# Kernel tuning notes

Measured on AMD Instinct MI355X. Metric: run time of the kernel, lower is better.

## Reference

```python
import jax, jax.numpy as jnp
import numpy as np

GRID = 64
AABB_MIN = np.array([-1.25, -1.55, -1.25], dtype=np.float32)
AABB_MAX = np.array([1.25, 0.95, 1.25], dtype=np.float32)
DENSITY_THRESH = 0.5


def setup_inputs() -> dict:
    key = jax.random.key(0)
    ks = jax.random.split(key, 12)
    N, S, H = 8192, 128, 64
    rays_o = jax.random.normal(ks[0], (N, 3), jnp.float32) * 0.1
    d = jax.random.normal(ks[1], (N, 3), jnp.float32)
    rays_d = d / jnp.sqrt(jnp.clip(jnp.sum(d * d, -1, keepdims=True), 1e-20))
    near = 0.05 + jax.random.uniform(ks[2], (N,), jnp.float32) * 0.5
    far = near + 2.0 + jax.random.uniform(ks[3], (N,), jnp.float32) * 0.5
    jitter = jax.random.uniform(ks[4], (N, S), jnp.float32)
    density_field = jax.random.uniform(ks[5], (GRID, GRID, GRID), jnp.float32)
    W1 = jax.random.normal(ks[6], (3, H), jnp.float32) * 0.5
    b1 = jnp.zeros((H,), jnp.float32)
    W2 = jax.random.normal(ks[7], (H, H), jnp.float32) * (1.0 / np.sqrt(H))
    b2 = jnp.zeros((H,), jnp.float32)
    Wsig = jax.random.normal(ks[8], (H, 1), jnp.float32) * (1.0 / np.sqrt(H))
    bsig = jnp.zeros((1,), jnp.float32)
    Wrgb = jax.random.normal(ks[9], (H, 3), jnp.float32) * (1.0 / np.sqrt(H))
    brgb = jnp.zeros((3,), jnp.float32)
    return {"rays_o": rays_o, "rays_d": rays_d, "near": near, "far": far,
            "jitter": jitter, "density_field": density_field,
            "W1": W1, "b1": b1, "W2": W2, "b2": b2,
            "Wsig": Wsig, "bsig": bsig, "Wrgb": Wrgb, "brgb": brgb}


def _render_train(rays_o, rays_d, near, far, jitter, density_field,
                  W1, b1, W2, b2, Wsig, bsig, Wrgb, brgb):
    N, S = jitter.shape
    step = (far - near) / S                                  # [N]
    offset = jnp.asarray(AABB_MIN)
    scale = jnp.asarray(AABB_MAX) - jnp.asarray(AABB_MIN)
    # uniform march (raymarch_train): z_i = near + i*step, zeroed where grid empty
    z = near[:, None] + jnp.arange(S, dtype=jnp.float32)[None, :] * step[:, None]  # [N,S]
    pts0 = rays_o[:, None, :] + z[..., None] * rays_d[:, None, :]                  # [N,S,3]
    u = (pts0 - offset) / scale
    idx = jnp.floor(u * GRID).astype(jnp.int32)
    inb = jnp.all((idx >= 0) & (idx < GRID), axis=-1)
    idxc = jnp.clip(idx, 0, GRID - 1)
    occ = density_field[idxc[..., 0], idxc[..., 1], idxc[..., 2]] > DENSITY_THRESH
    z_vals = jnp.where(occ & inb, z, 0.0)                    # [N,S]
    mask = z_vals > 0
    # stratified jitter (torch: z_vals + rand * step_size)
    z_vals = z_vals + jitter * step[:, None]
    pts = rays_o[:, None, :] + z_vals[..., None] * rays_d[:, None, :]  # [N,S,3]
    # radiance-field MLP (stand-in for `model(pts, None)`)
    h = jax.nn.relu(jnp.einsum('nsc,ch->nsh', pts, W1) + b1)
    h = jax.nn.relu(jnp.einsum('nsh,hk->nsk', h, W2) + b2)
    sigma = (jnp.einsum('nsh,ho->nso', h, Wsig) + bsig)[..., 0]        # [N,S]
    rgb = jax.nn.sigmoid(jnp.einsum('nsh,ho->nso', h, Wrgb) + brgb)    # [N,S,3]
    # torch fills masked-out samples with sigma=-1000, rgb=0
    sigma = jnp.where(mask, sigma, -1000.0)
    rgb = jnp.where(mask[..., None], rgb, 0.0)
    # composite
    dists = jnp.broadcast_to(step[:, None], sigma.shape)
    tau = jax.nn.relu(sigma) * dists
    alpha = 1.0 - jnp.exp(-tau)
    trans = jnp.concatenate([jnp.ones_like(alpha[..., :1]),
                             jnp.cumprod(1.0 - alpha + 1e-10, axis=-1)], axis=-1)
    w = alpha * trans[..., :-1]                              # [N,S]
    no_hit = trans[..., -1]
    color = jnp.sum(w[..., None] * rgb, axis=-2) + no_hit[..., None]   # bg_color=None -> white
    depth = jnp.sum(w * z_vals, axis=-1)
    return color, depth


def reference(rays_o, rays_d, near, far, jitter, density_field,
              W1, b1, W2, b2, Wsig, bsig, Wrgb, brgb):
    color, depth = _render_train(rays_o, rays_d, near, far, jitter, density_field,
                                 W1, b1, W2, b2, Wsig, bsig, Wrgb, brgb)
    return color
```

## Files before the change

kernel.cpp:

```cpp
#include <hip/hip_runtime.h>
#include <math.h>

#define S 128
#define H 64
#define RPB 8
#define SPB (RPB * S)
#define T 256

typedef __attribute__((ext_vector_type(8))) short bf16x8;
typedef __attribute__((ext_vector_type(4))) float f32x4;
#define MFMA16(a, b, c) __builtin_amdgcn_mfma_f32_16x16x32_bf16((a), (b), (c), 0, 0, 0)

__device__ __forceinline__ short f2bf(float x) {
    unsigned u = __float_as_uint(x);
    unsigned r = (u + 0x7fffu + ((u >> 16) & 1u)) >> 16;
    return (short)r;
}

__device__ __forceinline__ bool sample_mask(
    float ox, float oy, float oz, float dx, float dy, float dz,
    float nr, float step, int s, const float* __restrict__ density)
{
    const float z  = __fadd_rn(nr, __fmul_rn((float)s, step));
    const float px = __fadd_rn(ox, __fmul_rn(z, dx));
    const float py = __fadd_rn(oy, __fmul_rn(z, dy));
    const float pz = __fadd_rn(oz, __fmul_rn(z, dz));
    const float gx = floorf(__fmul_rn(__fdiv_rn(__fsub_rn(px, -1.25f), 2.5f), 64.0f));
    const float gy = floorf(__fmul_rn(__fdiv_rn(__fsub_rn(py, -1.55f), 2.5f), 64.0f));
    const float gz = floorf(__fmul_rn(__fdiv_rn(__fsub_rn(pz, -1.25f), 2.5f), 64.0f));
    const int ix = (int)gx, iy = (int)gy, iz = (int)gz;
    const bool inb = (ix >= 0) && (ix < 64) && (iy >= 0) && (iy < 64) &&
                     (iz >= 0) && (iz < 64);
    const int cx = min(max(ix, 0), 63);
    const int cy = min(max(iy, 0), 63);
    const int cz = min(max(iz, 0), 63);
    const float dval = density[(cx << 12) | (cy << 6) | cz];
    return inb && (dval > 0.5f);
}

__global__ __launch_bounds__(256)
void fused_mfma_kernel(const float* __restrict__ rays_o, const float* __restrict__ rays_d,
                       const float* __restrict__ nearv, const float* __restrict__ farv,
                       const float* __restrict__ jitter, const float* __restrict__ density,
                       const float* __restrict__ W1, const float* __restrict__ b1,
                       const float* __restrict__ W2, const float* __restrict__ b2,
                       const float* __restrict__ Wsig, const float* __restrict__ bsig,
                       const float* __restrict__ Wrgb, const float* __restrict__ brgb,
                       float* __restrict__ out, int N)
{
    __shared__ __align__(16) short sW2t[H * 72];
    __shared__ __align__(16) short hX[4][16 * 72];
    __shared__ unsigned short s_list[SPB];
    __shared__ float s_alpha[SPB];
    __shared__ float s_r[SPB], s_g[SPB], s_b[SPB];
    __shared__ int s_wcnt[4];
    __shared__ int s_wbase[4];

    const int tid  = threadIdx.x;
    const int lane = tid & 63;
    const int wv   = tid >> 6;
    const int blk  = blockIdx.x;
    const int mrow = lane & 15;
    const int quad = lane >> 4;

    for (int e = tid; e < H * H; e += T) {
        const int k = e >> 6, n = e & 63;
        sW2t[n * 72 + k] = f2bf(W2[e]);
    }

    const int lbase = tid * 4;
    const int gra   = blk * RPB + (lbase >> 7);
    unsigned int mybits = 0u;
    if (gra < N) {
        const float ox = rays_o[gra * 3 + 0], oy = rays_o[gra * 3 + 1], oz = rays_o[gra * 3 + 2];
        const float dx = rays_d[gra * 3 + 0], dy = rays_d[gra * 3 + 1], dz = rays_d[gra * 3 + 2];
        const float nr = nearv[gra];
        const float step = __fdiv_rn(__fsub_rn(farv[gra], nr), 128.0f);
        const int s0 = lbase & (S - 1);
        #pragma unroll
        for (int j = 0; j < 4; ++j) {
            const bool m = sample_mask(ox, oy, oz, dx, dy, dz, nr, step, s0 + j, density);
            if (m) {
                mybits |= (1u << j);
            } else {
                s_alpha[lbase + j] = 0.0f;
                s_r[lbase + j] = 0.0f;
                s_g[lbase + j] = 0.0f;
                s_b[lbase + j] = 0.0f;
            }
        }
    } else {
        #pragma unroll
        for (int j = 0; j < 4; ++j) {
            s_alpha[lbase + j] = 0.0f;
            s_r[lbase + j] = 0.0f;
            s_g[lbase + j] = 0.0f;
            s_b[lbase + j] = 0.0f;
        }
    }
    const int mycnt = __popc(mybits);
    int inc = mycnt;
    #pragma unroll
    for (int off = 1; off < 64; off <<= 1) {
        const int u = __shfl_up(inc, off, 64);
        if (lane >= off) inc += u;
    }
    if (lane == 63) s_wcnt[wv] = inc;
    __syncthreads();
    if (tid == 0) {
        int t0 = 0;
        #pragma unroll
        for (int i = 0; i < 4; ++i) { s_wbase[i] = t0; t0 += s_wcnt[i]; }
    }
    __syncthreads();
    int pos = s_wbase[wv] + (inc - mycnt);
    #pragma unroll
    for (int j = 0; j < 4; ++j) {
        if ((mybits >> j) & 1u) s_list[pos++] = (unsigned short)(lbase + j);
    }
    __syncthreads();
    const int K = s_wbase[3] + s_wcnt[3];

    bf16x8 w2f[4][2];
    #pragma unroll
    for (int nt = 0; nt < 4; ++nt) {
        #pragma unroll
        for (int ks = 0; ks < 2; ++ks) {
            w2f[nt][ks] = *(const bf16x8*)&sW2t[(mrow + 16 * nt) * 72 + 32 * ks + 8 * quad];
        }
    }
    bf16x8 w1f[4];
    #pragma unroll
    for (int nt = 0; nt < 4; ++nt) {
        bf16x8 f = {0, 0, 0, 0, 0, 0, 0, 0};
        if (quad == 0) {
            const int n = mrow + 16 * nt;
            f[0] = f2bf(W1[n]);
            f[1] = f2bf(W1[64 + n]);
            f[2] = f2bf(W1[128 + n]);
        }
        w1f[nt] = f;
    }
    bf16x8 a3f[2];
    #pragma unroll
    for (int ks = 0; ks < 2; ++ks) {
        bf16x8 f = {0, 0, 0, 0, 0, 0, 0, 0};
        if (mrow < 4) {
            #pragma unroll
            for (int j = 0; j < 8; ++j) {
                const int k = 32 * ks + 8 * quad + j;
                const float v = (mrow == 0) ? Wsig[k] : Wrgb[k * 3 + (mrow - 1)];
                f[j] = f2bf(v);
            }
        }
        a3f[ks] = f;
    }
    float b1v[4], b2v[4];
    #pragma unroll
    for (int nt = 0; nt < 4; ++nt) {
        b1v[nt] = b1[mrow + 16 * nt];
        b2v[nt] = b2[mrow + 16 * nt];
    }
    const float bsg = bsig[0];
    const float br0 = brgb[0], br1 = brgb[1], br2 = brgb[2];

    const f32x4 z4 = {0.f, 0.f, 0.f, 0.f};
    const int ntask = (K + 15) >> 4;
    short* const hb = &hX[wv][0];

    for (int t = wv; t < ntask; t += 4) {
        const int slot = (t << 4) + mrow;
        const bool valid = slot < K;
        const int id = s_list[valid ? slot : 0];
        const int r = blk * RPB + (id >> 7);
        const int s = id & (S - 1);
        const float nr = nearv[r];
        const float step = __fdiv_rn(__fsub_rn(farv[r], nr), 128.0f);
        const float zs = __fadd_rn(nr, __fmul_rn((float)s, step));
        const float zj = zs + jitter[blk * SPB + id] * step;
        const float qx = rays_o[r * 3 + 0] + zj * rays_d[r * 3 + 0];
        const float qy = rays_o[r * 3 + 1] + zj * rays_d[r * 3 + 1];
        const float qz = rays_o[r * 3 + 2] + zj * rays_d[r * 3 + 2];

        bf16x8 ah = {0, 0, 0, 0, 0, 0, 0, 0};
        if (quad == 0) { ah[0] = f2bf(qx); ah[1] = f2bf(qy); ah[2] = f2bf(qz); }
        #pragma unroll
        for (int nt = 0; nt < 4; ++nt) {
            const f32x4 c1 = MFMA16(ah, w1f[nt], z4);
            #pragma unroll
            for (int rg = 0; rg < 4; ++rg) {
                const float v = fmaxf(c1[rg] + b1v[nt], 0.0f);
                hb[(4 * quad + rg) * 72 + mrow + 16 * nt] = f2bf(v);
            }
        }

        bf16x8 a2_0 = *(const bf16x8*)&hb[mrow * 72 + 8 * quad];
        bf16x8 a2_1 = *(const bf16x8*)&hb[mrow * 72 + 32 + 8 * quad];
        #pragma unroll
        for (int nt = 0; nt < 4; ++nt) {
            const f32x4 c2 = MFMA16(a2_1, w2f[nt][1], MFMA16(a2_0, w2f[nt][0], z4));
            #pragma unroll
            for (int rg = 0; rg < 4; ++rg) {
                const float v = fmaxf(c2[rg] + b2v[nt], 0.0f);
                hb[(4 * quad + rg) * 72 + mrow + 16 * nt] = f2bf(v);
            }
        }

        bf16x8 b3_0 = *(const bf16x8*)&hb[mrow * 72 + 8 * quad];
        bf16x8 b3_1 = *(const bf16x8*)&hb[mrow * 72 + 32 + 8 * quad];
        const f32x4 c3 = MFMA16(a3f[1], b3_1, MFMA16(a3f[0], b3_0, z4));

        if (quad == 0 && valid) {
            const float sg = c3[0] + bsg;
            const float tau = fmaxf(sg, 0.0f) * step;
            s_alpha[id] = 1.0f - expf(-tau);
            s_r[id] = 1.0f / (1.0f + expf(-(c3[1] + br0)));
            s_g[id] = 1.0f / (1.0f + expf(-(c3[2] + br1)));
            s_b[id] = 1.0f / (1.0f + expf(-(c3[3] + br2)));
        }
    }
    __syncthreads();

    #pragma unroll
    for (int ri = wv; ri < RPB; ri += 4) {
        const int gr = blk * RPB + ri;
        if (gr >= N) break;
        const int b0 = ri * S + 2 * lane;
        const float2 a01 = *reinterpret_cast<const float2*>(&s_alpha[b0]);
        const float a0 = a01.x, a1 = a01.y;
        const float t0 = (1.0f - a0) + 1e-10f;
        const float t1 = (1.0f - a1) + 1e-10f;
        float v = t0 * t1;
        #pragma unroll
        for (int off = 1; off < 64; off <<= 1) {
            const float u = __shfl_up(v, off, 64);
            if (lane >= off) v *= u;
        }
        float excl = __shfl_up(v, 1, 64);
        if (lane == 0) excl = 1.0f;
        const float no_hit = __shfl(v, 63, 64);
        const float w0 = a0 * excl;
        const float w1 = a1 * (excl * t0);
        const float2 r01 = *reinterpret_cast<const float2*>(&s_r[b0]);
        const float2 g01 = *reinterpret_cast<const float2*>(&s_g[b0]);
        const float2 b01 = *reinterpret_cast<const float2*>(&s_b[b0]);
        float cr = w0 * r01.x + w1 * r01.y;
        float cg = w0 * g01.x + w1 * g01.y;
        float cb = w0 * b01.x + w1 * b01.y;
        #pragma unroll
        for (int off = 32; off >= 1; off >>= 1) {
            cr += __shfl_xor(cr, off, 64);
            cg += __shfl_xor(cg, off, 64);
            cb += __shfl_xor(cb, off, 64);
        }
        if (lane == 0) {
            out[gr * 3 + 0] = cr + no_hit;
            out[gr * 3 + 1] = cg + no_hit;
            out[gr * 3 + 2] = cb + no_hit;
        }
    }
}

extern "C" void kernel_launch(void* const* d_in, const int* in_sizes, int n_in,
                              void* d_out, int out_size, void* d_ws, size_t ws_size,
                              hipStream_t stream) {
    const float* rays_o  = (const float*)d_in[0];
    const float* rays_d  = (const float*)d_in[1];
    const float* nearv   = (const float*)d_in[2];
    const float* farv    = (const float*)d_in[3];
    const float* jitter  = (const float*)d_in[4];
    const float* density = (const float*)d_in[5];
    const float* W1      = (const float*)d_in[6];
    const float* b1      = (const float*)d_in[7];
    const float* W2      = (const float*)d_in[8];
    const float* b2      = (const float*)d_in[9];
    const float* Wsig    = (const float*)d_in[10];
    const float* bsig    = (const float*)d_in[11];
    const float* Wrgb    = (const float*)d_in[12];
    const float* brgb    = (const float*)d_in[13];
    float* out = (float*)d_out;

    const int N = in_sizes[2];

    fused_mfma_kernel<<<dim3((N + RPB - 1) / RPB), dim3(T), 0, stream>>>(
        rays_o, rays_d, nearv, farv, jitter, density,
        W1, b1, W2, b2, Wsig, bsig, Wrgb, brgb, out, N);
}
```

Baseline: 105.8 us.

## Cut LDS and register pressure, fold bias into MFMA, cache ray params in LDS

Overlays the W2 staging buffer with the r/g color arrays in a union to shrink LDS, and adds an occupancy hint of 5 blocks per SM via launch bounds. Per-ray origin, direction, near and step are loaded once into shared memory instead of being re-read from global memory per sample. The b1 bias is folded into the first MFMA through a constant-one input column. The code also switches to hardware bf16 conversion, fast exp and rcp intrinsics, and moves the zero-fill of masked samples after the weight preload. Fast math intrinsics and the occupancy cap may change accuracy slightly or cause register spills.

```diff
diff --git a/kernel.cpp b/kernel.cpp
--- a/kernel.cpp
+++ b/kernel.cpp
@@ -12,9 +12,8 @@
 #define MFMA16(a, b, c) __builtin_amdgcn_mfma_f32_16x16x32_bf16((a), (b), (c), 0, 0, 0)
 
 __device__ __forceinline__ short f2bf(float x) {
-    unsigned u = __float_as_uint(x);
-    unsigned r = (u + 0x7fffu + ((u >> 16) & 1u)) >> 16;
-    return (short)r;
+    __bf16 b = (__bf16)x;
+    return __builtin_bit_cast(short, b);
 }
 
 __device__ __forceinline__ bool sample_mask(
@@ -38,7 +37,7 @@
     return inb && (dval > 0.5f);
 }
 
-__global__ __launch_bounds__(256)
+__global__ __launch_bounds__(256, 5)
 void fused_mfma_kernel(const float* __restrict__ rays_o, const float* __restrict__ rays_d,
                        const float* __restrict__ nearv, const float* __restrict__ farv,
                        const float* __restrict__ jitter, const float* __restrict__ density,
@@ -48,13 +47,22 @@
                        const float* __restrict__ Wrgb, const float* __restrict__ brgb,
                        float* __restrict__ out, int N)
 {
-    __shared__ __align__(16) short sW2t[H * 72];
+    __shared__ __align__(16) union {
+        short w2t[H * 72];
+        float rg[2 * SPB];
+    } s_u;
     __shared__ __align__(16) short hX[4][16 * 72];
     __shared__ unsigned short s_list[SPB];
-    __shared__ float s_alpha[SPB];
-    __shared__ float s_r[SPB], s_g[SPB], s_b[SPB];
+    __shared__ __align__(16) float s_alpha[SPB];
+    __shared__ __align__(16) float s_bv[SPB];
+    __shared__ __align__(16) float s_ray[RPB][8];
     __shared__ int s_wcnt[4];
     __shared__ int s_wbase[4];
+
+    short* const sW2t = s_u.w2t;
+    float* const s_r  = s_u.rg;
+    float* const s_g  = s_u.rg + SPB;
+    float* const s_b  = s_bv;
 
     const int tid  = threadIdx.x;
     const int lane = tid & 63;
@@ -63,39 +71,40 @@
     const int mrow = lane & 15;
     const int quad = lane >> 4;
 
+    if (tid < RPB) {
+        const int gr = blk * RPB + tid;
+        float ox = 0.f, oy = 0.f, oz = 0.f, dx = 0.f, dy = 0.f, dz = 0.f,
+              nr = 0.f, st = 0.f;
+        if (gr < N) {
+            ox = rays_o[gr * 3 + 0]; oy = rays_o[gr * 3 + 1]; oz = rays_o[gr * 3 + 2];
+            dx = rays_d[gr * 3 + 0]; dy = rays_d[gr * 3 + 1]; dz = rays_d[gr * 3 + 2];
+            nr = nearv[gr];
+            st = __fdiv_rn(__fsub_rn(farv[gr], nr), 128.0f);
+        }
+        s_ray[tid][0] = ox; s_ray[tid][1] = oy; s_ray[tid][2] = oz; s_ray[tid][3] = dx;
+        s_ray[tid][4] = dy; s_ray[tid][5] = dz; s_ray[tid][6] = nr; s_ray[tid][7] = st;
+    }
     for (int e = tid; e < H * H; e += T) {
         const int k = e >> 6, n = e & 63;
         sW2t[n * 72 + k] = f2bf(W2[e]);
     }
+    __syncthreads();
 
     const int lbase = tid * 4;
-    const int gra   = blk * RPB + (lbase >> 7);
+    const int rloc  = lbase >> 7;
+    const int gra   = blk * RPB + rloc;
     unsigned int mybits = 0u;
-    if (gra < N) {
-        const float ox = rays_o[gra * 3 + 0], oy = rays_o[gra * 3 + 1], oz = rays_o[gra * 3 + 2];
-        const float dx = rays_d[gra * 3 + 0], dy = rays_d[gra * 3 + 1], dz = rays_d[gra * 3 + 2];
-        const float nr = nearv[gra];
-        const float step = __fdiv_rn(__fsub_rn(farv[gra], nr), 128.0f);
-        const int s0 = lbase & (S - 1);
-        #pragma unroll
-        for (int j = 0; j < 4; ++j) {
-            const bool m = sample_mask(ox, oy, oz, dx, dy, dz, nr, step, s0 + j, density);
-            if (m) {
-                mybits |= (1u << j);
-            } else {
-                s_alpha[lbase + j] = 0.0f;
-                s_r[lbase + j] = 0.0f;
-                s_g[lbase + j] = 0.0f;
-                s_b[lbase + j] = 0.0f;
+    {
+        const float4 rv0 = *reinterpret_cast<const float4*>(&s_ray[rloc][0]);
+        const float4 rv1 = *reinterpret_cast<const float4*>(&s_ray[rloc][4]);
+        if (gra < N) {
+            const int s0 = lbase & (S - 1);
+            #pragma unroll
+            for (int j = 0; j < 4; ++j) {
+                if (sample_mask(rv0.x, rv0.y, rv0.z, rv0.w, rv1.x, rv1.y,
+                                rv1.z, rv1.w, s0 + j, density))
+                    mybits |= (1u << j);
             }
-        }
-    } else {
-        #pragma unroll
-        for (int j = 0; j < 4; ++j) {
-            s_alpha[lbase + j] = 0.0f;
-            s_r[lbase + j] = 0.0f;
-            s_g[lbase + j] = 0.0f;
-            s_b[lbase + j] = 0.0f;
         }
     }
     const int mycnt = __popc(mybits);
@@ -106,20 +115,6 @@
         if (lane >= off) inc += u;
     }
     if (lane == 63) s_wcnt[wv] = inc;
-    __syncthreads();
-    if (tid == 0) {
-        int t0 = 0;
-        #pragma unroll
-        for (int i = 0; i < 4; ++i) { s_wbase[i] = t0; t0 += s_wcnt[i]; }
-    }
-    __syncthreads();
-    int pos = s_wbase[wv] + (inc - mycnt);
-    #pragma unroll
-    for (int j = 0; j < 4; ++j) {
-        if ((mybits >> j) & 1u) s_list[pos++] = (unsigned short)(lbase + j);
-    }
-    __syncthreads();
-    const int K = s_wbase[3] + s_wcnt[3];
 
     bf16x8 w2f[4][2];
     #pragma unroll
@@ -138,6 +133,7 @@
             f[0] = f2bf(W1[n]);
             f[1] = f2bf(W1[64 + n]);
             f[2] = f2bf(W1[128 + n]);
+            f[3] = f2bf(b1[n]);
         }
         w1f[nt] = f;
     }
@@ -155,68 +151,91 @@
         }
         a3f[ks] = f;
     }
-    float b1v[4], b2v[4];
-    #pragma unroll
-    for (int nt = 0; nt < 4; ++nt) {
-        b1v[nt] = b1[mrow + 16 * nt];
-        b2v[nt] = b2[mrow + 16 * nt];
-    }
+    float b2v[4];
+    #pragma unroll
+    for (int nt = 0; nt < 4; ++nt) b2v[nt] = b2[mrow + 16 * nt];
     const float bsg = bsig[0];
     const float br0 = brgb[0], br1 = brgb[1], br2 = brgb[2];
 
+    __syncthreads();
+    if (tid == 0) {
+        int t0 = 0;
+        #pragma unroll
+        for (int i = 0; i < 4; ++i) { s_wbase[i] = t0; t0 += s_wcnt[i]; }
+    }
+    __syncthreads();
+    int pos = s_wbase[wv] + (inc - mycnt);
+    #pragma unroll
+    for (int j = 0; j < 4; ++j) {
+        if ((mybits >> j) & 1u) {
+            s_list[pos++] = (unsigned short)(lbase + j);
+        } else {
+            s_alpha[lbase + j] = 0.0f;
+            s_r[lbase + j] = 0.0f;
+            s_g[lbase + j] = 0.0f;
+            s_b[lbase + j] = 0.0f;
+        }
+    }
+    const int K = s_wbase[3] + s_wcnt[3];
+    __syncthreads();
+
     const f32x4 z4 = {0.f, 0.f, 0.f, 0.f};
     const int ntask = (K + 15) >> 4;
-    short* const hb = &hX[wv][0];
+    short* const hb  = &hX[wv][0];
+    short* const hwr = hb + (4 * quad) * 72 + mrow;
+    const short* const hrd = hb + mrow * 72 + 8 * quad;
 
     for (int t = wv; t < ntask; t += 4) {
         const int slot = (t << 4) + mrow;
         const bool valid = slot < K;
         const int id = s_list[valid ? slot : 0];
-        const int r = blk * RPB + (id >> 7);
-        const int s = id & (S - 1);
-        const float nr = nearv[r];
-        const float step = __fdiv_rn(__fsub_rn(farv[r], nr), 128.0f);
+        const int ri = id >> 7;
+        const int s  = id & (S - 1);
+        const float4 rv0 = *reinterpret_cast<const float4*>(&s_ray[ri][0]);
+        const float4 rv1 = *reinterpret_cast<const float4*>(&s_ray[ri][4]);
+        const float nr = rv1.z, step = rv1.w;
         const float zs = __fadd_rn(nr, __fmul_rn((float)s, step));
         const float zj = zs + jitter[blk * SPB + id] * step;
-        const float qx = rays_o[r * 3 + 0] + zj * rays_d[r * 3 + 0];
-        const float qy = rays_o[r * 3 + 1] + zj * rays_d[r * 3 + 1];
-        const float qz = rays_o[r * 3 + 2] + zj * rays_d[r * 3 + 2];
+        const float qx = rv0.x + zj * rv0.w;
+        const float qy = rv0.y + zj * rv1.x;
+        const float qz = rv0.z + zj * rv1.y;
 
         bf16x8 ah = {0, 0, 0, 0, 0, 0, 0, 0};
-        if (quad == 0) { ah[0] = f2bf(qx); ah[1] = f2bf(qy); ah[2] = f2bf(qz); }
+        if (quad == 0) {
+            ah[0] = f2bf(qx); ah[1] = f2bf(qy); ah[2] = f2bf(qz);
+            ah[3] = (short)0x3F80;
+        }
         #pragma unroll
         for (int nt = 0; nt < 4; ++nt) {
             const f32x4 c1 = MFMA16(ah, w1f[nt], z4);
             #pragma unroll
             for (int rg = 0; rg < 4; ++rg) {
-                const float v = fmaxf(c1[rg] + b1v[nt], 0.0f);
-                hb[(4 * quad + rg) * 72 + mrow + 16 * nt] = f2bf(v);
+                hwr[rg * 72 + 16 * nt] = f2bf(fmaxf(c1[rg], 0.0f));
             }
         }
 
-        bf16x8 a2_0 = *(const bf16x8*)&hb[mrow * 72 + 8 * quad];
-        bf16x8 a2_1 = *(const bf16x8*)&hb[mrow * 72 + 32 + 8 * quad];
+        const bf16x8 a2_0 = *(const bf16x8*)(hrd);
+        const bf16x8 a2_1 = *(const bf16x8*)(hrd + 32);
         #pragma unroll
         for (int nt = 0; nt < 4; ++nt) {
             const f32x4 c2 = MFMA16(a2_1, w2f[nt][1], MFMA16(a2_0, w2f[nt][0], z4));
             #pragma unroll
             for (int rg = 0; rg < 4; ++rg) {
-                const float v = fmaxf(c2[rg] + b2v[nt], 0.0f);
-                hb[(4 * quad + rg) * 72 + mrow + 16 * nt] = f2bf(v);
+                hwr[rg * 72 + 16 * nt] = f2bf(fmaxf(c2[rg] + b2v[nt], 0.0f));
             }
         }
 
-        bf16x8 b3_0 = *(const bf16x8*)&hb[mrow * 72 + 8 * quad];
-        bf16x8 b3_1 = *(const bf16x8*)&hb[mrow * 72 + 32 + 8 * quad];
+        const bf16x8 b3_0 = *(const bf16x8*)(hrd);
+        const bf16x8 b3_1 = *(const bf16x8*)(hrd + 32);
         const f32x4 c3 = MFMA16(a3f[1], b3_1, MFMA16(a3f[0], b3_0, z4));
 
         if (quad == 0 && valid) {
             const float sg = c3[0] + bsg;
             const float tau = fmaxf(sg, 0.0f) * step;
-            s_alpha[id] = 1.0f - expf(-tau);
-            s_r[id] = 1.0f / (1.0f + expf(-(c3[1] + br0)));
-            s_g[id] = 1.0f / (1.0f + expf(-(c3[2] + br1)));
-            s_b[id] = 1.0f / (1.0f + expf(-(c3[3] + br2)));
+            s_alpha[id] = 1.0f - __expf(-tau);
+            s_r[id] = __builtin_amdgcn_rcpf(1.0f + __expf(-(c3[1] + br0)));
+            s_g[id] = __builtin_amdgcn_rcpf(1.0f + __expf(-(c3[2] + br1)));
+            s_b[id] = __builtin_amdgcn_rcpf(1.0f + __expf(-(c3[3] + br2)));
         }
     }
     __syncthreads();
```

New measurement: 102.4 us. 3.1% less time.
